# Performance work log

Measured on AMD Instinct MI355X. Metric: run time of the kernel, lower is better.

## Reference

```python
import jax, jax.numpy as jnp
import numpy as np

B, T = 8, 4096
EMBED_DIM = 128
ENGRAM_EMBED_DIM = 64
VOCAB_SIZES = [4096, 4096]
MAX_NGRAM = 3
NUM_HEADS = 2
N_STREAMS = 4
KERNEL = 4
TOTAL_NGRAMS = len(VOCAB_SIZES) * NUM_HEADS          # 4
INPUT_DIM = TOTAL_NGRAMS * ENGRAM_EMBED_DIM          # 256
TOTAL_SLOTS = sum(VOCAB_SIZES) * NUM_HEADS           # 16384


def setup_inputs() -> dict:
    key = jax.random.key(0)
    ks = jax.random.split(key, 10)
    x = jax.random.normal(ks[0], (B, T, N_STREAMS, EMBED_DIM), dtype=jnp.float32)
    input_ids = jax.random.randint(ks[1], (B, T), 0, 50257, dtype=jnp.int32)
    multipliers = jax.random.randint(ks[2], (MAX_NGRAM - 1, NUM_HEADS, MAX_NGRAM), 1, 10000, dtype=jnp.int32)
    embedding = jax.random.normal(ks[3], (TOTAL_SLOTS, ENGRAM_EMBED_DIM), dtype=jnp.float32) * 0.02
    val_W = jax.random.normal(ks[4], (EMBED_DIM, INPUT_DIM), dtype=jnp.float32) * 0.05
    val_b = jnp.zeros((EMBED_DIM,), jnp.float32)
    key_W = jax.random.normal(ks[5], (N_STREAMS, EMBED_DIM, INPUT_DIM), dtype=jnp.float32) * 0.05
    key_b = jnp.zeros((N_STREAMS, EMBED_DIM), jnp.float32)
    normq_w = jnp.ones((N_STREAMS, EMBED_DIM), jnp.float32)
    normk_w = jnp.ones((N_STREAMS, EMBED_DIM), jnp.float32)
    conv_w = jax.random.normal(ks[6], (N_STREAMS * EMBED_DIM, 1, KERNEL), dtype=jnp.float32) * 0.1
    convnorm_w = jnp.ones((N_STREAMS, EMBED_DIM), jnp.float32)
    return {"x": x, "input_ids": input_ids, "multipliers": multipliers,
            "embedding": embedding, "val_W": val_W, "val_b": val_b,
            "key_W": key_W, "key_b": key_b, "normq_w": normq_w,
            "normk_w": normk_w, "conv_w": conv_w, "convnorm_w": convnorm_w}


def rmsnorm(v, w):
    # torch nn.RMSNorm default eps = finfo(dtype).eps
    eps = jnp.finfo(v.dtype).eps
    return v * jax.lax.rsqrt(jnp.mean(v * v, axis=-1, keepdims=True) + eps) * w


def hash_ids_fn(input_ids, multipliers):
    padded = jnp.pad(input_ids, ((0, 0), (MAX_NGRAM - 1, 0)))            # [B, T+2]
    windows = jnp.stack([padded[:, i:i + T] for i in range(MAX_NGRAM)], axis=-1)  # [B,T,3]
    hashes = []
    for n_idx in range(MAX_NGRAM - 1):
        ngram_len = n_idx + 2
        grams = windows[:, :, MAX_NGRAM - ngram_len:]                    # [B,T,L]
        mults = multipliers[n_idx, :, :ngram_len]                        # [H,L]
        mixed = grams[:, :, None, :] * mults[None, None, :, :]           # [B,T,H,L]
        h = mixed[..., 0]
        for k in range(1, ngram_len):
            h = jnp.bitwise_xor(h, mixed[..., k])
        hashes.append(h % VOCAB_SIZES[n_idx])                            # [B,T,H]
    return jnp.concatenate(hashes, axis=2)                               # [B,T,4]


def engram_forward(x, input_ids, multipliers, embedding, val_W, val_b,
                   key_W, key_b, normq_w, normk_w, conv_w, convnorm_w):
    hids = hash_ids_fn(input_ids, multipliers)
    offsets = jnp.cumsum(jnp.array([0] + [v for v in VOCAB_SIZES for _ in range(NUM_HEADS)], jnp.int32))[:-1]
    ids = hids + offsets                                                 # [B,T,4]
    emb = embedding[ids].reshape(B, T, INPUT_DIM)                        # [B,T,256]
    v_base = emb @ val_W.T + val_b                                       # [B,T,128]
    k = rmsnorm(jnp.einsum('bte,gde->btgd', emb, key_W) + key_b, normk_w)  # [B,T,G,D]
    q = rmsnorm(x, normq_w)                                              # [B,T,G,D]
    score = jnp.sum(q * k, axis=-1, keepdims=True) / (EMBED_DIM ** 0.5)
    gates = jax.nn.sigmoid(score)                                        # [B,T,G,1]
    v_gated = v_base[:, :, None, :] * gates                              # [B,T,G,D]
    # ShortConv: per-chunk RMSNorm -> causal depthwise conv -> SiLU
    xn = rmsnorm(v_gated, convnorm_w).reshape(B, T, N_STREAMS * EMBED_DIM)
    x_bct = jnp.transpose(xn, (0, 2, 1))                                 # [B,C,T]
    x_bct = jnp.pad(x_bct, ((0, 0), (0, 0), (KERNEL - 1, 0)))            # causal left pad
    y_bct = jax.lax.conv_general_dilated(
        x_bct, conv_w, window_strides=(1,), padding='VALID',
        dimension_numbers=('NCH', 'OIH', 'NCH'),
        feature_group_count=N_STREAMS * EMBED_DIM)                       # [B,C,T]
    y = jax.nn.silu(y_bct)
    y = jnp.transpose(y, (0, 2, 1)).reshape(B, T, N_STREAMS, EMBED_DIM)
    return v_gated + y


def reference(x, input_ids, multipliers, embedding, val_W, val_b,
              key_W, key_b, normq_w, normk_w, conv_w, convnorm_w):
    return engram_forward(x, input_ids, multipliers, embedding, val_W, val_b,
                          key_W, key_b, normq_w, normk_w, conv_w, convnorm_w)
```

## Files before the change

### kernel.cpp

```cpp
#include <hip/hip_runtime.h>
#include <math.h>

#define EPS 1.1920928955078125e-07f

typedef __attribute__((ext_vector_type(8)))  short short8;
typedef __attribute__((ext_vector_type(4)))  short short4v;
typedef __attribute__((ext_vector_type(16))) float floatx16;

__device__ __forceinline__ float4 ld4(const float* __restrict__ p) { return *(const float4* __restrict__)p; }
__device__ __forceinline__ void   st4(float* __restrict__ p, float4 v) { *(float4* __restrict__)p = v; }

__device__ __forceinline__ unsigned short f2bf(float f) {
    union { float f; unsigned u; } v; v.f = f;
    unsigned r = v.u + 0x7fffu + ((v.u >> 16) & 1u);
    return (unsigned short)(r >> 16);
}

__global__ __launch_bounds__(256) void build_pack(const float* __restrict__ val_W,
                                                  const float* __restrict__ key_W,
                                                  const float* __restrict__ emb,
                                                  unsigned short* __restrict__ WbF,
                                                  unsigned short* __restrict__ ebf)
{
    int bid = blockIdx.x;
    if (bid < 80) {
        int idx  = bid * 256 + threadIdx.x;
        int lane = idx & 63;
        int ks   = (idx >> 6) & 15;
        int nt   = idx >> 10;
        int n = (nt << 5) + (lane & 31);
        int k = (ks << 4) + ((lane >> 5) << 3);
        const float* src = (n < 512) ? key_W + (size_t)n * 256 + k
                                     : val_W + (size_t)(n - 512) * 256 + k;
        float4 v0 = ld4(src), v1 = ld4(src + 4);
        unsigned short o[8] = { f2bf(v0.x), f2bf(v0.y), f2bf(v0.z), f2bf(v0.w),
                                f2bf(v1.x), f2bf(v1.y), f2bf(v1.z), f2bf(v1.w) };
        unsigned short* dst = WbF + (size_t)idx * 8;
        *(short4v*)dst       = *(short4v*)&o[0];
        *(short4v*)(dst + 4) = *(short4v*)&o[4];
    } else {
        int idx = (bid - 80) * 256 + threadIdx.x;
        const float* src = emb + ((size_t)idx << 3);
        float4 v0 = ld4(src), v1 = ld4(src + 4);
        unsigned short o[8] = { f2bf(v0.x), f2bf(v0.y), f2bf(v0.z), f2bf(v0.w),
                                f2bf(v1.x), f2bf(v1.y), f2bf(v1.z), f2bf(v1.w) };
        unsigned short* dst = ebf + ((size_t)idx << 3);
        *(short4v*)dst       = *(short4v*)&o[0];
        *(short4v*)(dst + 4) = *(short4v*)&o[4];
    }
}

__global__ __launch_bounds__(256, 4) void engram_gemm(
    const float* __restrict__ x,
    const int*   __restrict__ input_ids,
    const int*   __restrict__ mult,
    const unsigned short* __restrict__ ebf,
    const float* __restrict__ val_b,
    const float* __restrict__ key_b,
    const float* __restrict__ normq_w,
    const float* __restrict__ normk_w,
    const unsigned short* __restrict__ WbF,
    float* __restrict__ v_base,
    float* __restrict__ Gbuf,
    float* __restrict__ S2buf)
{
    __shared__ int   sids[32][4];
    __shared__ short A[32 * 260];
    __shared__ float D[32 * 130];

    const int tid  = threadIdx.x;
    const int tok0 = blockIdx.x << 5;

    if (tid < 32) {
        int token = tok0 + tid;
        int b = token >> 12, t = token & 4095;
        const int* row = input_ids + (b << 12);
        unsigned g2 = (unsigned)row[t];
        unsigned g1 = (t >= 1) ? (unsigned)row[t - 1] : 0u;
        unsigned g0 = (t >= 2) ? (unsigned)row[t - 2] : 0u;
        sids[tid][0] = (int)(((g1 * (unsigned)mult[0]) ^ (g2 * (unsigned)mult[1])) & 4095u);
        sids[tid][1] = (int)((((g1 * (unsigned)mult[3]) ^ (g2 * (unsigned)mult[4])) & 4095u) + 4096u);
        sids[tid][2] = (int)((((g0 * (unsigned)mult[6]) ^ (g1 * (unsigned)mult[7]) ^ (g2 * (unsigned)mult[8])) & 4095u) + 8192u);
        sids[tid][3] = (int)((((g0 * (unsigned)mult[9]) ^ (g1 * (unsigned)mult[10]) ^ (g2 * (unsigned)mult[11])) & 4095u) + 12288u);
    }
    __syncthreads();

    #pragma unroll
    for (int it = 0; it < 4; ++it) {
        int f = (it << 8) + tid;
        int token = f >> 5, ch = f & 31;
        const unsigned short* src = ebf + ((size_t)sids[token][ch >> 3] << 6) + ((ch & 7) << 3);
        short4v lo = *(const short4v*)src;
        short4v hi = *(const short4v*)(src + 4);
        short* dst = A + token * 260 + (ch << 3);
        *(short4v*)dst       = lo;
        *(short4v*)(dst + 4) = hi;
    }
    __syncthreads();

    const int lane = tid & 63;
    const int wv   = tid >> 6;
    const int half = lane >> 5;
    const int mrow = lane & 31;

    const short*  Ap = A + mrow * 260 + (half << 3);
    const float4* Bf = (const float4*)WbF + lane;

    const int ty = tid >> 4, tx = tid & 15;
    const int tx8 = tx << 3;
    const int colw = (wv << 5) + mrow;
    const int rb   = half << 2;

    for (int s = 0; s < 4; ++s) {
        const float* xp0 = x + ((((size_t)(tok0 + (ty << 1))     << 2) + s) << 7) + tx8;
        const float* xp1 = x + ((((size_t)(tok0 + (ty << 1) + 1) << 2) + s) << 7) + tx8;
        float4 xa0 = ld4(xp0), xb0 = ld4(xp0 + 4);
        float4 xa1 = ld4(xp1), xb1 = ld4(xp1 + 4);

        floatx16 acc;
        #pragma unroll
        for (int r = 0; r < 16; ++r) acc[r] = 0.f;
        const int nt = (s << 2) + wv;
        const float4* bp = Bf + ((size_t)(nt << 4) << 6);
        #pragma unroll 4
        for (int ks = 0; ks < 16; ++ks) {
            short4v al = *(const short4v*)(Ap + (ks << 4));
            short4v ah = *(const short4v*)(Ap + (ks << 4) + 4);
            short8 a = { al[0], al[1], al[2], al[3], ah[0], ah[1], ah[2], ah[3] };
            union { float4 f; short8 s8; } ub;
            ub.f = bp[(size_t)ks << 6];
            acc = __builtin_amdgcn_mfma_f32_32x32x16_bf16(a, ub.s8, acc, 0, 0, 0);
        }

        __syncthreads();
        #pragma unroll
        for (int r = 0; r < 16; ++r) {
            int row = (r & 3) + ((r >> 2) << 3) + rb;
            D[row * 130 + colw] = acc[r];
        }
        __syncthreads();

        const float* kbp = key_b   + (s << 7) + tx8;
        const float* nqp = normq_w + (s << 7) + tx8;
        const float* nkp = normk_w + (s << 7) + tx8;
        float4 kba = ld4(kbp), kbb = ld4(kbp + 4);
        float4 nqa = ld4(nqp), nqb = ld4(nqp + 4);
        float4 nka = ld4(nkp), nkb = ld4(nkp + 4);
        float kb[8] = {kba.x, kba.y, kba.z, kba.w, kbb.x, kbb.y, kbb.z, kbb.w};
        float nq[8] = {nqa.x, nqa.y, nqa.z, nqa.w, nqb.x, nqb.y, nqb.z, nqb.w};
        float nk[8] = {nka.x, nka.y, nka.z, nka.w, nkb.x, nkb.y, nkb.z, nkb.w};
        #pragma unroll
        for (int jj = 0; jj < 2; ++jj) {
            int t_loc = (ty << 1) + jj;
            int token = tok0 + t_loc;
            const float* dp = D + t_loc * 130 + tx8;
            float kr[8]; float ks2 = 0.f;
            #pragma unroll
            for (int m = 0; m < 8; ++m) { kr[m] = dp[m] + kb[m]; ks2 += kr[m] * kr[m]; }
            float xv[8];
            if (jj == 0) { xv[0]=xa0.x; xv[1]=xa0.y; xv[2]=xa0.z; xv[3]=xa0.w;
                           xv[4]=xb0.x; xv[5]=xb0.y; xv[6]=xb0.z; xv[7]=xb0.w; }
            else         { xv[0]=xa1.x; xv[1]=xa1.y; xv[2]=xa1.z; xv[3]=xa1.w;
                           xv[4]=xb1.x; xv[5]=xb1.y; xv[6]=xb1.z; xv[7]=xb1.w; }
            float xs2 = 0.f, dt = 0.f;
            #pragma unroll
            for (int m = 0; m < 8; ++m) { xs2 += xv[m] * xv[m]; dt += xv[m] * nq[m] * kr[m] * nk[m]; }
            #pragma unroll
            for (int off = 1; off < 16; off <<= 1) {
                ks2 += __shfl_xor(ks2, off);
                xs2 += __shfl_xor(xs2, off);
                dt  += __shfl_xor(dt,  off);
            }
            float sc = dt * rsqrtf(xs2 * (1.f / 128.f) + EPS)
                          * rsqrtf(ks2 * (1.f / 128.f) + EPS) * 0.08838834764831845f;
            float gate = 1.f / (1.f + __expf(-sc));
            if (tx == 0) Gbuf[(token << 2) + s] = gate;
        }
    }

    {
        floatx16 acc;
        #pragma unroll
        for (int r = 0; r < 16; ++r) acc[r] = 0.f;
        const int nt = 16 + wv;
        const float4* bp = Bf + ((size_t)(nt << 4) << 6);
        #pragma unroll 4
        for (int ks = 0; ks < 16; ++ks) {
            short4v al = *(const short4v*)(Ap + (ks << 4));
            short4v ah = *(const short4v*)(Ap + (ks << 4) + 4);
            short8 a = { al[0], al[1], al[2], al[3], ah[0], ah[1], ah[2], ah[3] };
            union { float4 f; short8 s8; } ub;
            ub.f = bp[(size_t)ks << 6];
            acc = __builtin_amdgcn_mfma_f32_32x32x16_bf16(a, ub.s8, acc, 0, 0, 0);
        }
        __syncthreads();
        #pragma unroll
        for (int r = 0; r < 16; ++r) {
            int row = (r & 3) + ((r >> 2) << 3) + rb;
            D[row * 130 + colw] = acc[r];
        }
        __syncthreads();

        const float* vbp = val_b + tx8;
        float4 vba = ld4(vbp), vbb = ld4(vbp + 4);
        float vb[8] = {vba.x, vba.y, vba.z, vba.w, vbb.x, vbb.y, vbb.z, vbb.w};
        #pragma unroll
        for (int jj = 0; jj < 2; ++jj) {
            int t_loc = (ty << 1) + jj;
            int token = tok0 + t_loc;
            const float* dp = D + t_loc * 130 + tx8;
            float v[8]; float s2 = 0.f;
            #pragma unroll
            for (int m = 0; m < 8; ++m) { v[m] = dp[m] + vb[m]; s2 += v[m] * v[m]; }
            #pragma unroll
            for (int off = 1; off < 16; off <<= 1) s2 += __shfl_xor(s2, off);
            float* vp = v_base + ((size_t)token << 7) + tx8;
            st4(vp,     make_float4(v[0], v[1], v[2], v[3]));
            st4(vp + 4, make_float4(v[4], v[5], v[6], v[7]));
            if (tx == 0) S2buf[token] = s2;
        }
    }
}

__global__ __launch_bounds__(256, 4) void engram_out(
    const float* __restrict__ v_base,
    const float* __restrict__ Gbuf,
    const float* __restrict__ S2buf,
    const float* __restrict__ conv_w,
    const float* __restrict__ convnorm_w,
    float* __restrict__ out)
{
    int idx  = blockIdx.x * 256 + threadIdx.x;
    int d4   = idx & 31;
    int sp   = (idx >> 5) & 1;
    int grp  = idx >> 6;
    int tg0  = grp << 2;
    int tsq0 = tg0 & 4095;
    int s0   = sp << 1;

    float v[7][4];
    float fw[7][2];
    float gq[4][2];
    #pragma unroll
    for (int j = 0; j < 7; ++j) {
        if (tsq0 + j >= 3) {
            int glob = tg0 - 3 + j;
            float4 vv = ld4(v_base + ((size_t)glob << 7) + (d4 << 2));
            v[j][0] = vv.x; v[j][1] = vv.y; v[j][2] = vv.z; v[j][3] = vv.w;
            float s2n = S2buf[glob] * (1.f / 128.f);
            #pragma unroll
            for (int q = 0; q < 2; ++q) {
                float g = Gbuf[(glob << 2) + s0 + q];
                fw[j][q] = g * rsqrtf(g * g * s2n + EPS);
                if (j >= 3) gq[j - 3][q] = g;
            }
        } else {
            #pragma unroll
            for (int i = 0; i < 4; ++i) v[j][i] = 0.f;
            fw[j][0] = 0.f; fw[j][1] = 0.f;
        }
    }

    float4 w[2][4];
    float  cw[2][4];
    #pragma unroll
    for (int q = 0; q < 2; ++q) {
        float4 c = ld4(convnorm_w + ((s0 + q) << 7) + (d4 << 2));
        cw[q][0] = c.x; cw[q][1] = c.y; cw[q][2] = c.z; cw[q][3] = c.w;
        #pragma unroll
        for (int i = 0; i < 4; ++i)
            w[q][i] = ld4(conv_w + (size_t)(((((s0 + q) << 7) + (d4 << 2) + i)) << 2));
    }

    #pragma unroll
    for (int t = 0; t < 4; ++t) {
        int glob = tg0 + t;
        #pragma unroll
        for (int q = 0; q < 2; ++q) {
            float o[4];
            #pragma unroll
            for (int i = 0; i < 4; ++i) {
                float a = w[q][i].x * v[t][i]     * fw[t][q]
                        + w[q][i].y * v[t + 1][i] * fw[t + 1][q]
                        + w[q][i].z * v[t + 2][i] * fw[t + 2][q]
                        + w[q][i].w * v[t + 3][i] * fw[t + 3][q];
                float y = a * cw[q][i];
                o[i] = v[t + 3][i] * gq[t][q] + y / (1.f + __expf(-y));
            }
            st4(out + ((size_t)((glob << 2) + s0 + q) << 7) + (d4 << 2),
                make_float4(o[0], o[1], o[2], o[3]));
        }
    }
}

extern "C" void kernel_launch(void* const* d_in, const int* in_sizes, int n_in,
                              void* d_out, int out_size, void* d_ws, size_t ws_size,
                              hipStream_t stream)
{
    const float* x          = (const float*)d_in[0];
    const int*   input_ids  = (const int*)d_in[1];
    const int*   mult       = (const int*)d_in[2];
    const float* embedding  = (const float*)d_in[3];
    const float* val_W      = (const float*)d_in[4];
    const float* val_b      = (const float*)d_in[5];
    const float* key_W      = (const float*)d_in[6];
    const float* key_b      = (const float*)d_in[7];
    const float* normq_w    = (const float*)d_in[8];
    const float* normk_w    = (const float*)d_in[9];
    const float* conv_w     = (const float*)d_in[10];
    const float* convnorm_w = (const float*)d_in[11];
    float* out = (float*)d_out;

    char* ws = (char*)d_ws;
    unsigned short* WbF = (unsigned short*)ws;
    unsigned short* ebf = (unsigned short*)(ws + 327680);
    float* v_base = (float*)(ws + 327680 + 2097152);
    float* Gbuf   = (float*)(ws + 327680 + 2097152 + 16777216);
    float* S2buf  = (float*)(ws + 327680 + 2097152 + 16777216 + 524288);

    build_pack<<<592, 256, 0, stream>>>(val_W, key_W, embedding, WbF, ebf);
    engram_gemm<<<1024, 256, 0, stream>>>(x, input_ids, mult, ebf, val_b, key_b,
                                          normq_w, normk_w, WbF, v_base, Gbuf, S2buf);
    engram_out<<<2048, 256, 0, stream>>>(v_base, Gbuf, S2buf, conv_w, convnorm_w, out);
}
```

Measured before the change: 164.1 us.

## Compute gate reductions directly from MFMA registers, removing LDS staging and barriers

Each wave now owns one stream and loops over its four column tiles, folding key bias, norms and the q·k dot product straight from the MFMA accumulators into per-row partial sums. These are then reduced with cross-lane shuffles, so the shared D tile and the paired __syncthreads around it go away. The value projection writes v_base directly from registers and sums row energy through a small shared partial array. In exchange, x is read with scalar strided loads per accumulator element instead of float4 loads, register pressure rises with 48 partial accumulators, and each row needs many more shuffle reductions.

```diff
diff --git a/kernel.cpp b/kernel.cpp
--- a/kernel.cpp
+++ b/kernel.cpp
@@ -66,7 +66,7 @@
 {
     __shared__ int   sids[32][4];
     __shared__ short A[32 * 260];
-    __shared__ float D[32 * 130];
+    __shared__ float S2part[4][32];
 
     const int tid  = threadIdx.x;
     const int tok0 = blockIdx.x << 5;
@@ -105,24 +105,70 @@
 
     const short*  Ap = A + mrow * 260 + (half << 3);
     const float4* Bf = (const float4*)WbF + lane;
-
-    const int ty = tid >> 4, tx = tid & 15;
-    const int tx8 = tx << 3;
-    const int colw = (wv << 5) + mrow;
-    const int rb   = half << 2;
-
-    for (int s = 0; s < 4; ++s) {
-        const float* xp0 = x + ((((size_t)(tok0 + (ty << 1))     << 2) + s) << 7) + tx8;
-        const float* xp1 = x + ((((size_t)(tok0 + (ty << 1) + 1) << 2) + s) << 7) + tx8;
-        float4 xa0 = ld4(xp0), xb0 = ld4(xp0 + 4);
-        float4 xa1 = ld4(xp1), xb1 = ld4(xp1 + 4);
-
+    const int     hb = half << 2;
+
+    {
+        const int s = wv;
+        float ks2[16], dts[16], xs2[16];
+        #pragma unroll
+        for (int r = 0; r < 16; ++r) { ks2[r] = 0.f; dts[r] = 0.f; xs2[r] = 0.f; }
+
+        #pragma unroll 1
+        for (int j = 0; j < 4; ++j) {
+            const int nt = (s << 2) + j;
+            const float4* bp = Bf + ((size_t)(nt << 4) << 6);
+            floatx16 acc;
+            #pragma unroll
+            for (int r = 0; r < 16; ++r) acc[r] = 0.f;
+            #pragma unroll
+            for (int ks = 0; ks < 16; ++ks) {
+                short4v al = *(const short4v*)(Ap + (ks << 4));
+                short4v ah = *(const short4v*)(Ap + (ks << 4) + 4);
+                short8 a = { al[0], al[1], al[2], al[3], ah[0], ah[1], ah[2], ah[3] };
+                union { float4 f; short8 s8; } ub;
+                ub.f = bp[(size_t)ks << 6];
+                acc = __builtin_amdgcn_mfma_f32_32x32x16_bf16(a, ub.s8, acc, 0, 0, 0);
+            }
+            const int dim = (j << 5) + mrow;
+            const float kb = key_b[(s << 7) + dim];
+            const float qk = normq_w[(s << 7) + dim] * normk_w[(s << 7) + dim];
+            #pragma unroll
+            for (int r = 0; r < 16; ++r) {
+                const int t = (r & 3) + ((r >> 2) << 3) + hb;
+                const float xval = x[((((size_t)(tok0 + t) << 2) + s) << 7) + dim];
+                const float kr = acc[r] + kb;
+                ks2[r] += kr * kr;
+                dts[r] += xval * kr * qk;
+                xs2[r] += xval * xval;
+            }
+        }
+
+        #pragma unroll
+        for (int r = 0; r < 16; ++r) {
+            float a2 = ks2[r], b2 = xs2[r], c2 = dts[r];
+            #pragma unroll
+            for (int off = 1; off < 32; off <<= 1) {
+                a2 += __shfl_xor(a2, off);
+                b2 += __shfl_xor(b2, off);
+                c2 += __shfl_xor(c2, off);
+            }
+            const float sc = c2 * rsqrtf(b2 * (1.f / 128.f) + EPS)
+                                * rsqrtf(a2 * (1.f / 128.f) + EPS) * 0.08838834764831845f;
+            const float gate = 1.f / (1.f + __expf(-sc));
+            if (mrow == 0) {
+                const int t = (r & 3) + ((r >> 2) << 3) + hb;
+                Gbuf[((tok0 + t) << 2) + s] = gate;
+            }
+        }
+    }
+
+    {
+        const int nt = 16 + wv;
+        const float4* bp = Bf + ((size_t)(nt << 4) << 6);
         floatx16 acc;
         #pragma unroll
         for (int r = 0; r < 16; ++r) acc[r] = 0.f;
-        const int nt = (s << 2) + wv;
-        const float4* bp = Bf + ((size_t)(nt << 4) << 6);
-        #pragma unroll 4
+        #pragma unroll
         for (int ks = 0; ks < 16; ++ks) {
             short4v al = *(const short4v*)(Ap + (ks << 4));
             short4v ah = *(const short4v*)(Ap + (ks << 4) + 4);
@@ -131,95 +177,22 @@
             ub.f = bp[(size_t)ks << 6];
             acc = __builtin_amdgcn_mfma_f32_32x32x16_bf16(a, ub.s8, acc, 0, 0, 0);
         }
-
-        __syncthreads();
+        const int dim = (wv << 5) + mrow;
+        const float vb = val_b[dim];
         #pragma unroll
         for (int r = 0; r < 16; ++r) {
-            int row = (r & 3) + ((r >> 2) << 3) + rb;
-            D[row * 130 + colw] = acc[r];
-        }
-        __syncthreads();
-
-        const float* kbp = key_b   + (s << 7) + tx8;
-        const float* nqp = normq_w + (s << 7) + tx8;
-        const float* nkp = normk_w + (s << 7) + tx8;
-        float4 kba = ld4(kbp), kbb = ld4(kbp + 4);
-        float4 nqa = ld4(nqp), nqb = ld4(nqp + 4);
-        float4 nka = ld4(nkp), nkb = ld4(nkp + 4);
-        float kb[8] = {kba.x, kba.y, kba.z, kba.w, kbb.x, kbb.y, kbb.z, kbb.w};
-        float nq[8] = {nqa.x, nqa.y, nqa.z, nqa.w, nqb.x, nqb.y, nqb.z, nqb.w};
-        float nk[8] = {nka.x, nka.y, nka.z, nka.w, nkb.x, nkb.y, nkb.z, nkb.w};
-        #pragma unroll
-        for (int jj = 0; jj < 2; ++jj) {
-            int t_loc = (ty << 1) + jj;
-            int token = tok0 + t_loc;
-            const float* dp = D + t_loc * 130 + tx8;
-            float kr[8]; float ks2 = 0.f;
-            #pragma unroll
-            for (int m = 0; m < 8; ++m) { kr[m] = dp[m] + kb[m]; ks2 += kr[m] * kr[m]; }
-            float xv[8];
-            if (jj == 0) { xv[0]=xa0.x; xv[1]=xa0.y; xv[2]=xa0.z; xv[3]=xa0.w;
-                           xv[4]=xb0.x; xv[5]=xb0.y; xv[6]=xb0.z; xv[7]=xb0.w; }
-            else         { xv[0]=xa1.x; xv[1]=xa1.y; xv[2]=xa1.z; xv[3]=xa1.w;
-                           xv[4]=xb1.x; xv[5]=xb1.y; xv[6]=xb1.z; xv[7]=xb1.w; }
-            float xs2 = 0.f, dt = 0.f;
-            #pragma unroll
-            for (int m = 0; m < 8; ++m) { xs2 += xv[m] * xv[m]; dt += xv[m] * nq[m] * kr[m] * nk[m]; }
-            #pragma unroll
-            for (int off = 1; off < 16; off <<= 1) {
-                ks2 += __shfl_xor(ks2, off);
-                xs2 += __shfl_xor(xs2, off);
-                dt  += __shfl_xor(dt,  off);
-            }
-            float sc = dt * rsqrtf(xs2 * (1.f / 128.f) + EPS)
-                          * rsqrtf(ks2 * (1.f / 128.f) + EPS) * 0.08838834764831845f;
-            float gate = 1.f / (1.f + __expf(-sc));
-            if (tx == 0) Gbuf[(token << 2) + s] = gate;
-        }
-    }
-
-    {
-        floatx16 acc;
-        #pragma unroll
-        for (int r = 0; r < 16; ++r) acc[r] = 0.f;
-        const int nt = 16 + wv;
-        const float4* bp = Bf + ((size_t)(nt << 4) << 6);
-        #pragma unroll 4
-        for (int ks = 0; ks < 16; ++ks) {
-            short4v al = *(const short4v*)(Ap + (ks << 4));
-            short4v ah = *(const short4v*)(Ap + (ks << 4) + 4);
-            short8 a = { al[0], al[1], al[2], al[3], ah[0], ah[1], ah[2], ah[3] };
-            union { float4 f; short8 s8; } ub;
-            ub.f = bp[(size_t)ks << 6];
-            acc = __builtin_amdgcn_mfma_f32_32x32x16_bf16(a, ub.s8, acc, 0, 0, 0);
-        }
-        __syncthreads();
-        #pragma unroll
-        for (int r = 0; r < 16; ++r) {
-            int row = (r & 3) + ((r >> 2) << 3) + rb;
-            D[row * 130 + colw] = acc[r];
-        }
-        __syncthreads();
-
-        const float* vbp = val_b + tx8;
-        float4 vba = ld4(vbp), vbb = ld4(vbp + 4);
-        float vb[8] = {vba.x, vba.y, vba.z, vba.w, vbb.x, vbb.y, vbb.z, vbb.w};
-        #pragma unroll
-        for (int jj = 0; jj < 2; ++jj) {
-            int t_loc = (ty << 1) + jj;
-            int token = tok0 + t_loc;
-            const float* dp = D + t_loc * 130 + tx8;
-            float v[8]; float s2 = 0.f;
-            #pragma unroll
-            for (int m = 0; m < 8; ++m) { v[m] = dp[m] + vb[m]; s2 += v[m] * v[m]; }
-            #pragma unroll
-            for (int off = 1; off < 16; off <<= 1) s2 += __shfl_xor(s2, off);
-            float* vp = v_base + ((size_t)token << 7) + tx8;
-            st4(vp,     make_float4(v[0], v[1], v[2], v[3]));
-            st4(vp + 4, make_float4(v[4], v[5], v[6], v[7]));
-            if (tx == 0) S2buf[token] = s2;
-        }
-    }
+            const int t = (r & 3) + ((r >> 2) << 3) + hb;
+            const float v = acc[r] + vb;
+            v_base[((size_t)(tok0 + t) << 7) + dim] = v;
+            float s2 = v * v;
+            #pragma unroll
+            for (int off = 1; off < 32; off <<= 1) s2 += __shfl_xor(s2, off);
+            if (mrow == 0) S2part[wv][t] = s2;
+        }
+    }
+    __syncthreads();
+    if (tid < 32)
+        S2buf[tok0 + tid] = S2part[0][tid] + S2part[1][tid] + S2part[2][tid] + S2part[3][tid];
 }
 
 __global__ __launch_bounds__(256, 4) void engram_out(
```

New measurement: 214.1 us. 1.31x slower.

## Split gemm kernel across stream pairs, shrink LDS with bf16 staging

Applied to the files above, without the earlier changes.

Each token tile is now handled by two blocks, each covering two of the four key streams, and only the second block computes the value projection. This doubles the grid and raises the occupancy hint. The key projection result is staged in LDS as bf16 instead of fp32, and the value path reuses the A buffer for its fp32 staging, which cuts shared memory per block. In exchange, the hash computation and embedding gather are repeated in both blocks, the two blocks do unequal work, and the key values lose precision before the norm.

```diff
diff --git a/kernel.cpp b/kernel.cpp
--- a/kernel.cpp
+++ b/kernel.cpp
@@ -14,6 +14,10 @@
     union { float f; unsigned u; } v; v.f = f;
     unsigned r = v.u + 0x7fffu + ((v.u >> 16) & 1u);
     return (unsigned short)(r >> 16);
+}
+__device__ __forceinline__ float bf2f(short s) {
+    union { unsigned u; float f; } v; v.u = ((unsigned)(unsigned short)s) << 16;
+    return v.f;
 }
 
 __global__ __launch_bounds__(256) void build_pack(const float* __restrict__ val_W,
@@ -50,7 +54,7 @@
     }
 }
 
-__global__ __launch_bounds__(256, 4) void engram_gemm(
+__global__ __launch_bounds__(256, 6) void engram_gemm(
     const float* __restrict__ x,
     const int*   __restrict__ input_ids,
     const int*   __restrict__ mult,
@@ -65,11 +69,12 @@
     float* __restrict__ S2buf)
 {
     __shared__ int   sids[32][4];
-    __shared__ short A[32 * 260];
-    __shared__ float D[32 * 130];
+    __shared__ short AD[32 * 260];
+    __shared__ short Dbf[32 * 132];
 
     const int tid  = threadIdx.x;
-    const int tok0 = blockIdx.x << 5;
+    const int part = blockIdx.x >> 10;
+    const int tok0 = (blockIdx.x & 1023) << 5;
 
     if (tid < 32) {
         int token = tok0 + tid;
@@ -92,7 +97,7 @@
         const unsigned short* src = ebf + ((size_t)sids[token][ch >> 3] << 6) + ((ch & 7) << 3);
         short4v lo = *(const short4v*)src;
         short4v hi = *(const short4v*)(src + 4);
-        short* dst = A + token * 260 + (ch << 3);
+        short* dst = AD + token * 260 + (ch << 3);
         *(short4v*)dst       = lo;
         *(short4v*)(dst + 4) = hi;
     }
@@ -103,7 +108,7 @@
     const int half = lane >> 5;
     const int mrow = lane & 31;
 
-    const short*  Ap = A + mrow * 260 + (half << 3);
+    const short*  Ap = AD + mrow * 260 + (half << 3);
     const float4* Bf = (const float4*)WbF + lane;
 
     const int ty = tid >> 4, tx = tid & 15;
@@ -111,7 +116,10 @@
     const int colw = (wv << 5) + mrow;
     const int rb   = half << 2;
 
-    for (int s = 0; s < 4; ++s) {
+    const int sbase = part << 1;
+    #pragma unroll 1
+    for (int si = 0; si < 2; ++si) {
+        const int s = sbase + si;
         const float* xp0 = x + ((((size_t)(tok0 + (ty << 1))     << 2) + s) << 7) + tx8;
         const float* xp1 = x + ((((size_t)(tok0 + (ty << 1) + 1) << 2) + s) << 7) + tx8;
         float4 xa0 = ld4(xp0), xb0 = ld4(xp0 + 4);
@@ -136,7 +144,7 @@
         #pragma unroll
         for (int r = 0; r < 16; ++r) {
             int row = (r & 3) + ((r >> 2) << 3) + rb;
-            D[row * 130 + colw] = acc[r];
+            Dbf[row * 132 + colw] = (short)f2bf(acc[r]);
         }
         __syncthreads();
 
@@ -147,16 +155,20 @@
         float4 nqa = ld4(nqp), nqb = ld4(nqp + 4);
         float4 nka = ld4(nkp), nkb = ld4(nkp + 4);
         float kb[8] = {kba.x, kba.y, kba.z, kba.w, kbb.x, kbb.y, kbb.z, kbb.w};
-        float nq[8] = {nqa.x, nqa.y, nqa.z, nqa.w, nqb.x, nqb.y, nqb.z, nqb.w};
-        float nk[8] = {nka.x, nka.y, nka.z, nka.w, nkb.x, nkb.y, nkb.z, nkb.w};
+        float qk[8] = {nqa.x * nka.x, nqa.y * nka.y, nqa.z * nka.z, nqa.w * nka.w,
+                       nqb.x * nkb.x, nqb.y * nkb.y, nqb.z * nkb.z, nqb.w * nkb.w};
         #pragma unroll
         for (int jj = 0; jj < 2; ++jj) {
             int t_loc = (ty << 1) + jj;
             int token = tok0 + t_loc;
-            const float* dp = D + t_loc * 130 + tx8;
+            const short* dpb = Dbf + t_loc * 132 + tx8;
+            short4v d0 = *(const short4v*)dpb;
+            short4v d1 = *(const short4v*)(dpb + 4);
             float kr[8]; float ks2 = 0.f;
             #pragma unroll
-            for (int m = 0; m < 8; ++m) { kr[m] = dp[m] + kb[m]; ks2 += kr[m] * kr[m]; }
+            for (int m = 0; m < 4; ++m) { kr[m]     = bf2f(d0[m]) + kb[m];     ks2 += kr[m] * kr[m]; }
+            #pragma unroll
+            for (int m = 0; m < 4; ++m) { kr[m + 4] = bf2f(d1[m]) + kb[m + 4]; ks2 += kr[m + 4] * kr[m + 4]; }
             float xv[8];
             if (jj == 0) { xv[0]=xa0.x; xv[1]=xa0.y; xv[2]=xa0.z; xv[3]=xa0.w;
                            xv[4]=xb0.x; xv[5]=xb0.y; xv[6]=xb0.z; xv[7]=xb0.w; }
@@ -164,7 +176,7 @@
                            xv[4]=xb1.x; xv[5]=xb1.y; xv[6]=xb1.z; xv[7]=xb1.w; }
             float xs2 = 0.f, dt = 0.f;
             #pragma unroll
-            for (int m = 0; m < 8; ++m) { xs2 += xv[m] * xv[m]; dt += xv[m] * nq[m] * kr[m] * nk[m]; }
+            for (int m = 0; m < 8; ++m) { xs2 += xv[m] * xv[m]; dt += xv[m] * kr[m] * qk[m]; }
             #pragma unroll
             for (int off = 1; off < 16; off <<= 1) {
                 ks2 += __shfl_xor(ks2, off);
@@ -178,7 +190,7 @@
         }
     }
 
-    {
+    if (part == 1) {
         floatx16 acc;
         #pragma unroll
         for (int r = 0; r < 16; ++r) acc[r] = 0.f;
@@ -194,6 +206,7 @@
             acc = __builtin_amdgcn_mfma_f32_32x32x16_bf16(a, ub.s8, acc, 0, 0, 0);
         }
         __syncthreads();
+        float* D = (float*)AD;
         #pragma unroll
         for (int r = 0; r < 16; ++r) {
             int row = (r & 3) + ((r >> 2) << 3) + rb;
@@ -319,7 +332,7 @@
     float* S2buf  = (float*)(ws + 327680 + 2097152 + 16777216 + 524288);
 
     build_pack<<<592, 256, 0, stream>>>(val_W, key_W, embedding, WbF, ebf);
-    engram_gemm<<<1024, 256, 0, stream>>>(x, input_ids, mult, ebf, val_b, key_b,
+    engram_gemm<<<2048, 256, 0, stream>>>(x, input_ids, mult, ebf, val_b, key_b,
                                           normq_w, normk_w, WbF, v_base, Gbuf, S2buf);
     engram_out<<<2048, 256, 0, stream>>>(v_base, Gbuf, S2buf, conv_w, convnorm_w, out);
 }
```

Result: slower. 174.3 us (+6.2%).
